# Optimization experiments

Hardware: AMD Instinct MI355X
Metric: run time of the kernel (lower is better)

## Reference

```python
import jax, jax.numpy as jnp
import numpy as np

B, S, D = 8, 2048, 512
EPS = float(jnp.finfo(jnp.float32).eps)  # torch RMSNorm eps=None -> finfo eps


def rmsnorm(x, w):
    var = jnp.mean(jnp.square(x), axis=-1, keepdims=True)
    return x * jax.lax.rsqrt(var + EPS) * w


def setup_inputs() -> dict:
    key = jax.random.key(0)
    ks = jax.random.split(key, 9)
    x = jax.random.normal(ks[0], (B, S, D), dtype=jnp.float32)
    q_expl = jax.random.normal(ks[1], (B, S, D), dtype=jnp.float32)
    k_expl = jax.random.normal(ks[2], (B, S, D), dtype=jnp.float32)
    # parameters (torch Linear: y = x @ W^T + b; store W already transposed [in, out])
    sc1 = 1.0 / np.sqrt(D)
    W1 = jax.random.uniform(ks[3], (D, 2 * D), jnp.float32, -sc1, sc1)
    b1 = jax.random.uniform(ks[4], (2 * D,), jnp.float32, -sc1, sc1)
    W2 = jax.random.uniform(ks[5], (D, D), jnp.float32, -sc1, sc1)
    b2 = jax.random.uniform(ks[6], (D,), jnp.float32, -sc1, sc1)
    norm1_w = jnp.ones((D,), jnp.float32)
    norm2_w = jnp.ones((D,), jnp.float32)
    return {"x": x, "q_expl": q_expl, "k_expl": k_expl,
            "W1": W1, "b1": b1, "W2": W2, "b2": b2,
            "norm1_w": norm1_w, "norm2_w": norm2_w}


def reference(x, q_expl, k_expl, W1, b1, W2, b2, norm1_w, norm2_w):
    d = x.shape[-1]
    # single-head attention: scores [B,S,S]
    scores = jnp.einsum('bqd,bkd->bqk', q_expl, k_expl) / jnp.sqrt(jnp.float32(d))
    attn = jax.nn.softmax(scores, axis=-1)
    attn_out = jnp.einsum('bqk,bkd->bqd', attn, x)
    # dropout is identity in eval mode
    h = rmsnorm(x + attn_out, norm1_w)
    # GeGLU FFN: Linear(D->2D), chunk, gelu(x1)*x2, Linear(D->D)
    proj = h @ W1 + b1
    x1, x2 = jnp.split(proj, 2, axis=-1)
    g = jax.nn.gelu(x1, approximate=False) * x2
    ff = g @ W2 + b2
    return rmsnorm(h + ff, norm2_w)
```

## Files before the change

### kernel.cpp

```cpp
#include <hip/hip_runtime.h>
#include <math.h>

static constexpr float EPS_F = 1.1920929e-07f;
static constexpr float SCL   = 0.044194173824159216f;

typedef __attribute__((ext_vector_type(8))) short  short8;
typedef __attribute__((ext_vector_type(4))) float  floatx4;

__device__ __forceinline__ float4 ld4(const float* p){ return *(const float4*)p; }
__device__ __forceinline__ ushort f2bf(float f){
  union { float f; unsigned u; } v; v.f = f;
  return (ushort)((v.u + 0x7FFFu + ((v.u >> 16) & 1u)) >> 16);
}
__device__ __forceinline__ float bf2f(ushort h){
  union { unsigned u; float f; } v; v.u = ((unsigned)h) << 16;
  return v.f;
}
#define MFMA16(A,B,C) __builtin_amdgcn_mfma_f32_16x16x32_bf16((A),(B),(C),0,0,0)

__device__ __forceinline__ void gld16(void* lds, const void* g){
  __builtin_amdgcn_global_load_lds(
      (const __attribute__((address_space(1))) unsigned int*)g,
      (__attribute__((address_space(3))) unsigned int*)lds, 16, 0, 0);
}


__global__ __launch_bounds__(256)
void prep(const float* __restrict__ q, const float* __restrict__ k,
          const float* __restrict__ x, const float* __restrict__ W1,
          const float* __restrict__ W2,
          ushort* __restrict__ Qb, ushort* __restrict__ Kb,
          ushort* __restrict__ XT, ushort* __restrict__ W1T,
          ushort* __restrict__ W2T)
{
  const int bi = blockIdx.x, t = threadIdx.x;
  if (bi < 8192){
    const size_t i4 = ((size_t)bi*256 + t)*4;
    float4 v = ld4(q + i4);
    ushort4 o;
    o.x=f2bf(v.x*SCL); o.y=f2bf(v.y*SCL); o.z=f2bf(v.z*SCL); o.w=f2bf(v.w*SCL);
    *(ushort4*)(Qb + i4) = o;
    float4 u = ld4(k + i4);
    o.x=f2bf(u.x); o.y=f2bf(u.y); o.z=f2bf(u.z); o.w=f2bf(u.w);
    *(ushort4*)(Kb + i4) = o;
    return;
  }
  const float* in; ushort* out; int R, C, c0, r0; size_t boff;
  if (bi < 10240){
    const int id = bi - 8192;
    in = x; out = XT; R = 2048; C = 512;
    boff = (size_t)(id >> 8) * R * C;
    c0 = (id & 7)*64; r0 = ((id >> 3) & 31)*64;
  } else if (bi < 10368){
    const int id = bi - 10240;
    in = W1; out = W1T; R = 512; C = 1024; boff = 0;
    c0 = (id & 15)*64; r0 = (id >> 4)*64;
  } else {
    const int id = bi - 10368;
    in = W2; out = W2T; R = 512; C = 512; boff = 0;
    c0 = (id & 7)*64; r0 = (id >> 3)*64;
  }
  __shared__ __align__(16) ushort tile[64*68];
#pragma unroll
  for (int it = 0; it < 4; ++it){
    int f = t + it*256, r = f >> 4, c4 = f & 15;
    float4 v = ld4(in + boff + (size_t)(r0+r)*C + c0 + c4*4);
    ushort4 o; o.x=f2bf(v.x); o.y=f2bf(v.y); o.z=f2bf(v.z); o.w=f2bf(v.w);
    *(ushort4*)&tile[r*68 + c4*4] = o;
  }
  __syncthreads();
#pragma unroll
  for (int it = 0; it < 4; ++it){
    int f = t + it*256, c = f >> 4, q4 = f & 15;
    ushort4 o;
    o.x = tile[(q4*4+0)*68 + c];
    o.y = tile[(q4*4+1)*68 + c];
    o.z = tile[(q4*4+2)*68 + c];
    o.w = tile[(q4*4+3)*68 + c];
    *(ushort4*)(out + boff + (size_t)(c0+c)*R + r0 + q4*4) = o;
  }
}

__global__ __launch_bounds__(512)
void qk3(const ushort* __restrict__ Qbf, const ushort* __restrict__ Kbf,
         ushort* __restrict__ scores, float* __restrict__ rowsum)
{
  extern __shared__ __align__(16) ushort smem[];
  const int t = threadIdx.x, lane = t & 63, w = t >> 6;
  const int id = blockIdx.x;
  const int b = id & 7, s = id >> 3;
  const int m0 = (s & 7) * 256, n0 = (s >> 3) * 256;
  const ushort* Ab = Qbf + ((size_t)b*2048 + m0)*512;
  const ushort* Bb = Kbf + ((size_t)b*2048 + n0)*512;
  const int wr = w >> 2, wc = w & 3;
  const int l15 = lane & 15, quad = lane >> 4;
  const int swk = ((l15 >> 1) & 3) * 8;
  const int rl  = lane >> 2;
  const int cl  = (lane & 3) ^ ((lane >> 3) & 3);
  const int aofb = (wr*128 + l15)*32 + (quad*8 ^ swk);
  const int bofb = (wc*64  + l15)*32 + (quad*8 ^ swk);

  floatx4 acc[8][4];
#pragma unroll
  for (int i = 0; i < 8; ++i)
#pragma unroll
    for (int j = 0; j < 4; ++j) acc[i][j] = (floatx4){0.f,0.f,0.f,0.f};

  auto stage = [&](int dstE, const ushort* gsrc, int kt){
#pragma unroll
    for (int r = 0; r < 2; ++r)
      gld16(smem + dstE + w*1024 + r*512,
            gsrc + (size_t)(w*32 + r*16 + rl)*512 + kt*32 + cl*8);
  };

  const int NT = 16;
  stage(0,             Ab, 0);
  stage(16384,         Bb, 0);
  stage(16384 + 8192,  Bb, 1);
  asm volatile("s_waitcnt vmcnt(2)" ::: "memory");
  __builtin_amdgcn_s_barrier();

  short8 af[4], bfr[4];
  for (int kt = 0; kt < NT; ++kt){
    const int cur = kt & 1;
    const ushort* A  = smem + cur*8192;
    const ushort* Bt = smem + 16384 + cur*8192;
#pragma unroll
    for (int n = 0; n < 4; ++n) bfr[n] = *(const short8*)&Bt[bofb + n*512];
#pragma unroll
    for (int m = 0; m < 4; ++m) af[m]  = *(const short8*)&A[aofb + m*512];
    if (kt+1 < NT) stage((cur^1)*8192, Ab, kt+1);
    __builtin_amdgcn_s_barrier();
    asm volatile("s_waitcnt lgkmcnt(0)" ::: "memory");
    __builtin_amdgcn_sched_barrier(0);
    __builtin_amdgcn_s_setprio(1);
#pragma unroll
    for (int m = 0; m < 4; ++m)
#pragma unroll
      for (int n = 0; n < 4; ++n)
        acc[m][n] = MFMA16(af[m], bfr[n], acc[m][n]);
    __builtin_amdgcn_s_setprio(0);
    __builtin_amdgcn_s_barrier();
#pragma unroll
    for (int m = 0; m < 4; ++m) af[m] = *(const short8*)&A[aofb + (4+m)*512];
    if (kt+2 < NT) stage(16384 + cur*8192, Bb, kt+2);
    __builtin_amdgcn_s_barrier();
    asm volatile("s_waitcnt lgkmcnt(0)" ::: "memory");
    __builtin_amdgcn_sched_barrier(0);
    __builtin_amdgcn_s_setprio(1);
#pragma unroll
    for (int m = 0; m < 4; ++m)
#pragma unroll
      for (int n = 0; n < 4; ++n)
        acc[4+m][n] = MFMA16(af[m], bfr[n], acc[4+m][n]);
    __builtin_amdgcn_s_setprio(0);
    if (kt + 2 < NT) asm volatile("s_waitcnt vmcnt(2)" ::: "memory");
    else             asm volatile("s_waitcnt vmcnt(0)" ::: "memory");
    __builtin_amdgcn_s_barrier();
  }

  ushort* sb = scores + (size_t)b*2048*2048;
#pragma unroll
  for (int m = 0; m < 8; ++m){
    const int rm = m0 + wr*128 + m*16 + quad*4;
    float rs[4] = {0.f,0.f,0.f,0.f};
#pragma unroll
    for (int n = 0; n < 4; ++n){
      const int cn = n0 + wc*64 + n*16 + l15;
#pragma unroll
      for (int r = 0; r < 4; ++r){
        float e = __expf(acc[m][n][r]);
        ushort eb = f2bf(e);
        sb[(size_t)(rm + r)*2048 + cn] = eb;
        rs[r] += bf2f(eb);
      }
    }
#pragma unroll
    for (int r = 0; r < 4; ++r){
      float p2 = rs[r];
      p2 += __shfl_xor(p2, 1); p2 += __shfl_xor(p2, 2);
      p2 += __shfl_xor(p2, 4); p2 += __shfl_xor(p2, 8);
      if (l15 == 0)
        atomicAdd(&rowsum[(size_t)b*2048 + rm + r], p2);
    }
  }
}

__global__ __launch_bounds__(512)
void pv8(const ushort* __restrict__ P, const ushort* __restrict__ XT,
         const float* __restrict__ rowsum, ushort* __restrict__ attn)
{
  extern __shared__ __align__(16) ushort smem[];
  const int t = threadIdx.x, lane = t & 63, w = t >> 6;
  const int id = blockIdx.x;
  const int b = id & 7, s = id >> 3;
  const int m0 = (s >> 2) * 256;
  const int n0 = (s & 3) * 128;
  const ushort* Pb = P  + ((size_t)b*2048 + m0)*2048;
  const ushort* Xb = XT + ((size_t)b*512  + n0)*2048;
  const int wr = w >> 1, wc = w & 1;
  const int l15 = lane & 15, quad = lane >> 4;
  const int c0  = (quad ^ (l15 & 7)) * 8;
  const int srow = lane >> 3;
  const int skc  = ((lane & 7) ^ srow) * 8;

  floatx4 acc[4][4];
#pragma unroll
  for (int i = 0; i < 4; ++i)
#pragma unroll
    for (int j = 0; j < 4; ++j) acc[i][j] = (floatx4){0.f,0.f,0.f,0.f};

  auto stageA = [&](int buf, int kt, int h){
    ushort* base = smem + buf*24576 + h*8192;
#pragma unroll
    for (int r = 0; r < 2; ++r){
      const int rw = r*8 + w;
      gld16(base + rw*512,
            Pb + (size_t)(h*128 + rw*8 + srow)*2048 + kt*64 + skc);
    }
  };
  auto stageB = [&](int buf, int kt){
    ushort* base = smem + buf*24576 + 16384;
#pragma unroll
    for (int r = 0; r < 2; ++r){
      const int rw = r*8 + w;
      gld16(base + rw*512,
            Xb + (size_t)(rw*8 + srow)*2048 + kt*64 + skc);
    }
  };

  stageA(0, 0, 0);
  stageA(0, 0, 1);
  stageB(0, 0);
  stageB(1, 1);
  asm volatile("s_waitcnt vmcnt(2)" ::: "memory");
  __builtin_amdgcn_s_barrier();

  short8 af[2][2], bfr[4][2];
  const int NT = 32;

  for (int kt = 0; kt < NT; ++kt){
    const int cur = kt & 1;
    const ushort* A  = smem + cur*24576;
    const ushort* Bt = A + 16384;

#pragma unroll
    for (int ni = 0; ni < 4; ++ni)
#pragma unroll
      for (int ks = 0; ks < 2; ++ks)
        bfr[ni][ks] = *(const short8*)
          &Bt[(wc*64 + ni*16 + l15)*64 + (c0 ^ (ks*32))];
#pragma unroll
    for (int mi = 0; mi < 2; ++mi)
#pragma unroll
      for (int ks = 0; ks < 2; ++ks)
        af[mi][ks] = *(const short8*)
          &A[(wr*64 + mi*16 + l15)*64 + (c0 ^ (ks*32))];
    if (kt+1 < NT) stageA(cur^1, kt+1, 0);
    __builtin_amdgcn_s_barrier();
    asm volatile("s_waitcnt lgkmcnt(0)" ::: "memory");
    __builtin_amdgcn_sched_barrier(0);
    __builtin_amdgcn_s_setprio(1);
#pragma unroll
    for (int mi = 0; mi < 2; ++mi)
#pragma unroll
      for (int ni = 0; ni < 4; ++ni)
#pragma unroll
        for (int ks = 0; ks < 2; ++ks)
          acc[mi][ni] = MFMA16(af[mi][ks], bfr[ni][ks], acc[mi][ni]);
    __builtin_amdgcn_s_setprio(0);
    __builtin_amdgcn_s_barrier();

#pragma unroll
    for (int mi = 0; mi < 2; ++mi)
#pragma unroll
      for (int ks = 0; ks < 2; ++ks)
        af[mi][ks] = *(const short8*)
          &A[(wr*64 + (2+mi)*16 + l15)*64 + (c0 ^ (ks*32))];
    if (kt+1 < NT) stageA(cur^1, kt+1, 1);
    if (kt+2 < NT) stageB(cur, kt+2);
    __builtin_amdgcn_s_barrier();
    asm volatile("s_waitcnt lgkmcnt(0)" ::: "memory");
    __builtin_amdgcn_sched_barrier(0);
    __builtin_amdgcn_s_setprio(1);
#pragma unroll
    for (int mi = 0; mi < 2; ++mi)
#pragma unroll
      for (int ni = 0; ni < 4; ++ni)
#pragma unroll
        for (int ks = 0; ks < 2; ++ks)
          acc[2+mi][ni] = MFMA16(af[mi][ks], bfr[ni][ks], acc[2+mi][ni]);
    __builtin_amdgcn_s_setprio(0);
    if (kt + 2 < NT) asm volatile("s_waitcnt vmcnt(2)" ::: "memory");
    else             asm volatile("s_waitcnt vmcnt(0)" ::: "memory");
    __builtin_amdgcn_s_barrier();
  }

  ushort* ab = attn + (size_t)b*2048*512;
#pragma unroll
  for (int m = 0; m < 4; ++m){
    const int rm = m0 + wr*64 + m*16 + quad*4;
    float inv[4];
#pragma unroll
    for (int r = 0; r < 4; ++r)
      inv[r] = 1.0f / rowsum[(size_t)b*2048 + rm + r];
#pragma unroll
    for (int n = 0; n < 4; ++n){
      const int cn = n0 + wc*64 + n*16 + l15;
#pragma unroll
      for (int r = 0; r < 4; ++r)
        ab[(size_t)(rm + r)*512 + cn] = f2bf(acc[m][n][r] * inv[r]);
    }
  }
}

__global__ __launch_bounds__(256)
void res_rms1(const float* __restrict__ x, const float* __restrict__ n1w,
              ushort* __restrict__ ah)
{
  const int wid = threadIdx.x >> 6, lane = threadIdx.x & 63;
  const size_t row = (size_t)blockIdx.x*4 + wid;
  ushort* ar = ah + row*512;
  const float* xr = x + row*512;
  ushort4 a0 = *(const ushort4*)&ar[lane*8];
  ushort4 a1 = *(const ushort4*)&ar[lane*8 + 4];
  float4 x0 = ld4(xr + lane*8), x1 = ld4(xr + lane*8 + 4);
  float h[8];
  h[0]=x0.x+bf2f(a0.x); h[1]=x0.y+bf2f(a0.y); h[2]=x0.z+bf2f(a0.z); h[3]=x0.w+bf2f(a0.w);
  h[4]=x1.x+bf2f(a1.x); h[5]=x1.y+bf2f(a1.y); h[6]=x1.z+bf2f(a1.z); h[7]=x1.w+bf2f(a1.w);
  float ss = 0.f;
#pragma unroll
  for (int e=0;e<8;++e) ss += h[e]*h[e];
#pragma unroll
  for (int s=1;s<64;s<<=1) ss += __shfl_xor(ss, s);
  const float rr = rsqrtf(ss*(1.0f/512.0f) + EPS_F);
  ushort4 o0, o1;
  o0.x=f2bf(h[0]*rr*n1w[lane*8+0]); o0.y=f2bf(h[1]*rr*n1w[lane*8+1]);
  o0.z=f2bf(h[2]*rr*n1w[lane*8+2]); o0.w=f2bf(h[3]*rr*n1w[lane*8+3]);
  o1.x=f2bf(h[4]*rr*n1w[lane*8+4]); o1.y=f2bf(h[5]*rr*n1w[lane*8+5]);
  o1.z=f2bf(h[6]*rr*n1w[lane*8+6]); o1.w=f2bf(h[7]*rr*n1w[lane*8+7]);
  *(ushort4*)&ar[lane*8]     = o0;
  *(ushort4*)&ar[lane*8 + 4] = o1;
}

__global__ __launch_bounds__(512, 4)
void ffn2(const ushort* __restrict__ hbf, const ushort* __restrict__ W1T,
          const float* __restrict__ b1, ushort* __restrict__ gbuf)
{
  extern __shared__ __align__(16) ushort smem[];
  const int t = threadIdx.x, lane = t & 63, w = t >> 6;
  const int id = blockIdx.x;
  const int xcd = id & 7, sl = id >> 3;
  const int m0 = (xcd*8 + (sl >> 3)) * 256;
  const int n0 = (sl & 7) * 64;
  const ushort* Ab = hbf + (size_t)m0*512;
  const int wr = w >> 1, wc = w & 1;
  const int l15 = lane & 15, quad = lane >> 4;
  const int rl = lane >> 2;
  const int cl = (lane & 3) ^ ((lane >> 3) & 3);
  const int sw = ((l15 >> 1) & 3) * 8;
  int aoff[4], boff[4];
#pragma unroll
  for (int m = 0; m < 4; ++m)
    aoff[m] = ((wr*64 + m*16 + l15)*32 + quad*8) ^ sw;
#pragma unroll
  for (int n = 0; n < 4; ++n)
    boff[n] = ((wc*64 + n*16 + l15)*32 + quad*8) ^ sw;
  const size_t aS0 = (size_t)(w*16 + rl)*512 + cl*8;
  const size_t aS1 = aS0 + (size_t)128*512;
  const int br = w*16 + rl;
  const int bgrow = ((br >> 5) & 1)*512 + n0 + (br >> 6)*32 + (br & 31);
  const size_t bS0 = (size_t)bgrow*512 + cl*8;
  const int aD = w*512, bD = 16384 + w*512;

  floatx4 acc[4][4];
#pragma unroll
  for (int i = 0; i < 4; ++i)
#pragma unroll
    for (int j = 0; j < 4; ++j) acc[i][j] = (floatx4){0.f,0.f,0.f,0.f};

  const int NT = 16;
  gld16(smem + aD,        Ab + aS0);
  gld16(smem + 4096 + aD, Ab + aS1);
  gld16(smem + bD,        W1T + bS0);
  gld16(smem + 4096 + bD, W1T + bS0 + 32);
  asm volatile("s_waitcnt vmcnt(1)" ::: "memory");
  __builtin_amdgcn_s_barrier();

  short8 af[2], bfr[4];
  for (int kt = 0; kt < NT; ++kt){
    const int cur = kt & 1;
    const ushort* A  = smem + cur*8192;
    const ushort* Bt = smem + 16384 + cur*4096;
#pragma unroll
    for (int n = 0; n < 4; ++n) bfr[n] = *(const short8*)&Bt[boff[n]];
#pragma unroll
    for (int m = 0; m < 2; ++m) af[m] = *(const short8*)&A[aoff[m]];
    if (kt+1 < NT){
      ushort* d = smem + (cur^1)*8192;
      const size_t ko = (size_t)(kt+1)*32;
      gld16(d + aD,        Ab + aS0 + ko);
      gld16(d + 4096 + aD, Ab + aS1 + ko);
    }
    __builtin_amdgcn_s_barrier();
    asm volatile("s_waitcnt lgkmcnt(0)" ::: "memory");
    __builtin_amdgcn_sched_barrier(0);
    __builtin_amdgcn_s_setprio(1);
#pragma unroll
    for (int m = 0; m < 2; ++m)
#pragma unroll
      for (int n = 0; n < 4; ++n)
        acc[m][n] = MFMA16(af[m], bfr[n], acc[m][n]);
    __builtin_amdgcn_s_setprio(0);
    __builtin_amdgcn_s_barrier();
#pragma unroll
    for (int m = 0; m < 2; ++m) af[m] = *(const short8*)&A[aoff[2+m]];
    if (kt+2 < NT)
      gld16(smem + cur*4096 + bD, W1T + bS0 + (size_t)(kt+2)*32);
    __builtin_amdgcn_s_barrier();
    asm volatile("s_waitcnt lgkmcnt(0)" ::: "memory");
    __builtin_amdgcn_sched_barrier(0);
    __builtin_amdgcn_s_setprio(1);
#pragma unroll
    for (int m = 0; m < 2; ++m)
#pragma unroll
      for (int n = 0; n < 4; ++n)
        acc[2+m][n] = MFMA16(af[m], bfr[n], acc[2+m][n]);
    __builtin_amdgcn_s_setprio(0);
    if (kt + 2 < NT) asm volatile("s_waitcnt vmcnt(1)" ::: "memory");
    else             asm volatile("s_waitcnt vmcnt(0)" ::: "memory");
    __builtin_amdgcn_s_barrier();
  }

#pragma unroll
  for (int m = 0; m < 4; ++m){
#pragma unroll
    for (int n = 0; n < 2; ++n){
      const int col = n0 + wc*32 + n*16 + l15;
      const float bb1 = b1[col], bb2 = b1[512 + col];
#pragma unroll
      for (int r = 0; r < 4; ++r){
        const int row = m0 + wr*64 + m*16 + quad*4 + r;
        float x1 = acc[m][n][r]     + bb1;
        float x2 = acc[m][n+2][r]   + bb2;
        float gl = 0.5f*x1*(1.0f + erff(x1*0.70710678118654752f));
        gbuf[(size_t)row*512 + col] = f2bf(gl*x2);
      }
    }
  }
}

__global__ __launch_bounds__(512, 4)
void ff2(const ushort* __restrict__ gb, const ushort* __restrict__ W2T,
         ushort* __restrict__ ff)
{
  extern __shared__ __align__(16) ushort smem[];
  const int t = threadIdx.x, lane = t & 63, w = t >> 6;
  const int id = blockIdx.x;
  const int xcd = id & 7, sl = id >> 3;
  const int m0 = (xcd*8 + (sl >> 2)) * 256;
  const int n0 = (sl & 3) * 128;
  const ushort* Ab = gb  + (size_t)m0*512;
  const ushort* Bb = W2T + (size_t)n0*512;
  const int wr = w >> 1, wc = w & 1;
  const int l15 = lane & 15, quad = lane >> 4;
  const int rl = lane >> 2;
  const int cl = (lane & 3) ^ ((lane >> 3) & 3);
  const int sw = ((l15 >> 1) & 3) * 8;
  int aoff[4], boff[4];
#pragma unroll
  for (int m = 0; m < 4; ++m)
    aoff[m] = ((wr*64 + m*16 + l15)*32 + quad*8) ^ sw;
#pragma unroll
  for (int n = 0; n < 4; ++n)
    boff[n] = ((wc*64 + n*16 + l15)*32 + quad*8) ^ sw;
  const size_t aS0 = (size_t)(w*16 + rl)*512 + cl*8;
  const size_t aS1 = aS0 + (size_t)128*512;
  const size_t bS0 = (size_t)(w*16 + rl)*512 + cl*8;
  const int aD = w*512, bD = 16384 + w*512;

  floatx4 acc[4][4];
#pragma unroll
  for (int i = 0; i < 4; ++i)
#pragma unroll
    for (int j = 0; j < 4; ++j) acc[i][j] = (floatx4){0.f,0.f,0.f,0.f};

  const int NT = 16;
  gld16(smem + aD,        Ab + aS0);
  gld16(smem + 4096 + aD, Ab + aS1);
  gld16(smem + bD,        Bb + bS0);
  gld16(smem + 4096 + bD, Bb + bS0 + 32);
  asm volatile("s_waitcnt vmcnt(1)" ::: "memory");
  __builtin_amdgcn_s_barrier();

  short8 af[2], bfr[4];
  for (int kt = 0; kt < NT; ++kt){
    const int cur = kt & 1;
    const ushort* A  = smem + cur*8192;
    const ushort* Bt = smem + 16384 + cur*4096;
#pragma unroll
    for (int n = 0; n < 4; ++n) bfr[n] = *(const short8*)&Bt[boff[n]];
#pragma unroll
    for (int m = 0; m < 2; ++m) af[m] = *(const short8*)&A[aoff[m]];
    if (kt+1 < NT){
      ushort* d = smem + (cur^1)*8192;
      const size_t ko = (size_t)(kt+1)*32;
      gld16(d + aD,        Ab + aS0 + ko);
      gld16(d + 4096 + aD, Ab + aS1 + ko);
    }
    __builtin_amdgcn_s_barrier();
    asm volatile("s_waitcnt lgkmcnt(0)" ::: "memory");
    __builtin_amdgcn_sched_barrier(0);
    __builtin_amdgcn_s_setprio(1);
#pragma unroll
    for (int m = 0; m < 2; ++m)
#pragma unroll
      for (int n = 0; n < 4; ++n)
        acc[m][n] = MFMA16(af[m], bfr[n], acc[m][n]);
    __builtin_amdgcn_s_setprio(0);
    __builtin_amdgcn_s_barrier();
#pragma unroll
    for (int m = 0; m < 2; ++m) af[m] = *(const short8*)&A[aoff[2+m]];
    if (kt+2 < NT)
      gld16(smem + cur*4096 + bD, Bb + bS0 + (size_t)(kt+2)*32);
    __builtin_amdgcn_s_barrier();
    asm volatile("s_waitcnt lgkmcnt(0)" ::: "memory");
    __builtin_amdgcn_sched_barrier(0);
    __builtin_amdgcn_s_setprio(1);
#pragma unroll
    for (int m = 0; m < 2; ++m)
#pragma unroll
      for (int n = 0; n < 4; ++n)
        acc[2+m][n] = MFMA16(af[m], bfr[n], acc[2+m][n]);
    __builtin_amdgcn_s_setprio(0);
    if (kt + 2 < NT) asm volatile("s_waitcnt vmcnt(1)" ::: "memory");
    else             asm volatile("s_waitcnt vmcnt(0)" ::: "memory");
    __builtin_amdgcn_s_barrier();
  }

#pragma unroll
  for (int m = 0; m < 4; ++m){
    const int rm = m0 + wr*64 + m*16 + quad*4;
#pragma unroll
    for (int n = 0; n < 4; ++n){
      const int cn = n0 + wc*64 + n*16 + l15;
#pragma unroll
      for (int r = 0; r < 4; ++r)
        ff[(size_t)(rm + r)*512 + cn] = f2bf(acc[m][n][r]);
    }
  }
}

__global__ __launch_bounds__(256)
void res_rms2(const ushort* __restrict__ hbf, const ushort* __restrict__ ff,
              const float* __restrict__ b2, const float* __restrict__ n2w,
              float* __restrict__ out)
{
  const int wid = threadIdx.x >> 6, lane = threadIdx.x & 63;
  const size_t row = (size_t)blockIdx.x*4 + wid;
  const ushort* hr = hbf + row*512;
  const ushort* fr = ff  + row*512;
  ushort4 h0 = *(const ushort4*)&hr[lane*8];
  ushort4 h1 = *(const ushort4*)&hr[lane*8 + 4];
  ushort4 f0 = *(const ushort4*)&fr[lane*8];
  ushort4 f1 = *(const ushort4*)&fr[lane*8 + 4];
  float4 bb0 = ld4(b2 + lane*8), bb1 = ld4(b2 + lane*8 + 4);
  float y[8];
  y[0]=bf2f(h0.x)+bf2f(f0.x)+bb0.x; y[1]=bf2f(h0.y)+bf2f(f0.y)+bb0.y;
  y[2]=bf2f(h0.z)+bf2f(f0.z)+bb0.z; y[3]=bf2f(h0.w)+bf2f(f0.w)+bb0.w;
  y[4]=bf2f(h1.x)+bf2f(f1.x)+bb1.x; y[5]=bf2f(h1.y)+bf2f(f1.y)+bb1.y;
  y[6]=bf2f(h1.z)+bf2f(f1.z)+bb1.z; y[7]=bf2f(h1.w)+bf2f(f1.w)+bb1.w;
  float ss = 0.f;
#pragma unroll
  for (int e=0;e<8;++e) ss += y[e]*y[e];
#pragma unroll
  for (int s=1;s<64;s<<=1) ss += __shfl_xor(ss, s);
  const float rr = rsqrtf(ss*(1.0f/512.0f) + EPS_F);
  float4 w0 = ld4(n2w + lane*8), w1 = ld4(n2w + lane*8 + 4);
  float* orow = out + row*512;
  float4 o0, o1;
  o0.x=y[0]*rr*w0.x; o0.y=y[1]*rr*w0.y; o0.z=y[2]*rr*w0.z; o0.w=y[3]*rr*w0.w;
  o1.x=y[4]*rr*w1.x; o1.y=y[5]*rr*w1.y; o1.z=y[6]*rr*w1.z; o1.w=y[7]*rr*w1.w;
  *(float4*)(orow + lane*8)     = o0;
  *(float4*)(orow + lane*8 + 4) = o1;
}

extern "C" void kernel_launch(void* const* d_in, const int* in_sizes, int n_in,
                              void* d_out, int out_size, void* d_ws, size_t ws_size,
                              hipStream_t stream)
{
  const float* x   = (const float*)d_in[0];
  const float* q   = (const float*)d_in[1];
  const float* k   = (const float*)d_in[2];
  const float* W1  = (const float*)d_in[3];
  const float* b1  = (const float*)d_in[4];
  const float* W2  = (const float*)d_in[5];
  const float* b2  = (const float*)d_in[6];
  const float* n1w = (const float*)d_in[7];
  const float* n2w = (const float*)d_in[8];
  float* out = (float*)d_out;

  ushort* scoresP = (ushort*)d_ws;
  ushort* XT  = scoresP + (size_t)8*2048*2048;
  ushort* Qbf = XT  + (size_t)8*512*2048;
  ushort* Kbf = Qbf + (size_t)8*2048*512;
  ushort* W1T = Kbf + (size_t)8*2048*512;
  ushort* W2T = W1T + (size_t)1024*512;
  float*  rowsum = (float*)(W2T + (size_t)512*512);
  ushort* attn = Qbf;
  ushort* hbf  = Qbf;
  ushort* gbuf = Kbf;
  ushort* ffb  = scoresP;

  hipMemsetAsync(rowsum, 0, (size_t)8*2048*sizeof(float), stream);
  prep     <<<dim3(10432),  256, 0, stream>>>(q, k, x, W1, W2, Qbf, Kbf, XT, W1T, W2T);
  qk3      <<<dim3(512),    512, 65536, stream>>>(Qbf, Kbf, scoresP, rowsum);
  pv8      <<<dim3(256),    512, 98304, stream>>>(scoresP, XT, rowsum, attn);
  res_rms1 <<<dim3(4096),   256, 0, stream>>>(x, n1w, hbf);
  ffn2     <<<dim3(512),    512, 49152, stream>>>(hbf, W1T, b1, gbuf);
  ff2      <<<dim3(256),    512, 49152, stream>>>(gbuf, W2T, ffb);
  res_rms2 <<<dim3(4096),   256, 0, stream>>>(hbf, ffb, b2, n2w, out);
}
```

Baseline: 302.8 us.

## Retile QK kernel to 256x128 blocks with 64-wide K steps and XOR swizzle

Rewrites the QK^T scores kernel to use 256x128 output tiles per block (1024 blocks instead of 512), a 4x2 wave layout, and 64-element K steps with a new XOR-swizzled shared-memory layout. Each step now issues two MFMAs per fragment pair and halves the number of K iterations, cutting barriers per unit of work. The change doubles the block count and raises LDS to 96KB, which may limit occupancy. It also lowers A/B operand reuse per block, since more Q rows are reloaded across the extra N tiles.

```diff
diff --git a/kernel.cpp b/kernel.cpp
--- a/kernel.cpp
+++ b/kernel.cpp
@@ -82,77 +82,109 @@
 }
 
 __global__ __launch_bounds__(512)
-void qk3(const ushort* __restrict__ Qbf, const ushort* __restrict__ Kbf,
+void qk5(const ushort* __restrict__ Qbf, const ushort* __restrict__ Kbf,
          ushort* __restrict__ scores, float* __restrict__ rowsum)
 {
   extern __shared__ __align__(16) ushort smem[];
   const int t = threadIdx.x, lane = t & 63, w = t >> 6;
   const int id = blockIdx.x;
   const int b = id & 7, s = id >> 3;
-  const int m0 = (s & 7) * 256, n0 = (s >> 3) * 256;
+  const int m0 = (s & 7) * 256;
+  const int n0 = (s >> 3) * 128;
   const ushort* Ab = Qbf + ((size_t)b*2048 + m0)*512;
   const ushort* Bb = Kbf + ((size_t)b*2048 + n0)*512;
-  const int wr = w >> 2, wc = w & 3;
+  const int wr = w >> 1, wc = w & 1;
   const int l15 = lane & 15, quad = lane >> 4;
-  const int swk = ((l15 >> 1) & 3) * 8;
-  const int rl  = lane >> 2;
-  const int cl  = (lane & 3) ^ ((lane >> 3) & 3);
-  const int aofb = (wr*128 + l15)*32 + (quad*8 ^ swk);
-  const int bofb = (wc*64  + l15)*32 + (quad*8 ^ swk);
-
-  floatx4 acc[8][4];
-#pragma unroll
-  for (int i = 0; i < 8; ++i)
+  const int c0  = (quad ^ (l15 & 7)) * 8;
+  const int srow = lane >> 3;
+  const int skc  = ((lane & 7) ^ srow) * 8;
+
+  floatx4 acc[4][4];
+#pragma unroll
+  for (int i = 0; i < 4; ++i)
 #pragma unroll
     for (int j = 0; j < 4; ++j) acc[i][j] = (floatx4){0.f,0.f,0.f,0.f};
 
-  auto stage = [&](int dstE, const ushort* gsrc, int kt){
-#pragma unroll
-    for (int r = 0; r < 2; ++r)
-      gld16(smem + dstE + w*1024 + r*512,
-            gsrc + (size_t)(w*32 + r*16 + rl)*512 + kt*32 + cl*8);
+  auto stageA = [&](int buf, int kt, int h){
+    ushort* base = smem + buf*24576 + h*8192;
+#pragma unroll
+    for (int r = 0; r < 2; ++r){
+      const int rw = r*8 + w;
+      gld16(base + rw*512,
+            Ab + (size_t)(h*128 + rw*8 + srow)*512 + kt*64 + skc);
+    }
   };
-
-  const int NT = 16;
-  stage(0,             Ab, 0);
-  stage(16384,         Bb, 0);
-  stage(16384 + 8192,  Bb, 1);
+  auto stageB = [&](int buf, int kt){
+    ushort* base = smem + buf*24576 + 16384;
+#pragma unroll
+    for (int r = 0; r < 2; ++r){
+      const int rw = r*8 + w;
+      gld16(base + rw*512,
+            Bb + (size_t)(rw*8 + srow)*512 + kt*64 + skc);
+    }
+  };
+
+  stageA(0, 0, 0);
+  stageA(0, 0, 1);
+  stageB(0, 0);
+  stageB(1, 1);
   asm volatile("s_waitcnt vmcnt(2)" ::: "memory");
   __builtin_amdgcn_s_barrier();
 
-  short8 af[4], bfr[4];
+  short8 af[2][2], bfr[4][2];
+  const int NT = 8;
+
   for (int kt = 0; kt < NT; ++kt){
     const int cur = kt & 1;
-    const ushort* A  = smem + cur*8192;
-    const ushort* Bt = smem + 16384 + cur*8192;
-#pragma unroll
-    for (int n = 0; n < 4; ++n) bfr[n] = *(const short8*)&Bt[bofb + n*512];
-#pragma unroll
-    for (int m = 0; m < 4; ++m) af[m]  = *(const short8*)&A[aofb + m*512];
-    if (kt+1 < NT) stage((cur^1)*8192, Ab, kt+1);
-    __builtin_amdgcn_s_barrier();
-    asm volatile("s_waitcnt lgkmcnt(0)" ::: "memory");
-    __builtin_amdgcn_sched_barrier(0);
-    __builtin_amdgcn_s_setprio(1);
-#pragma unroll
-    for (int m = 0; m < 4; ++m)
-#pragma unroll
-      for (int n = 0; n < 4; ++n)
-        acc[m][n] = MFMA16(af[m], bfr[n], acc[m][n]);
-    __builtin_amdgcn_s_setprio(0);
-    __builtin_amdgcn_s_barrier();
-#pragma unroll
-    for (int m = 0; m < 4; ++m) af[m] = *(const short8*)&A[aofb + (4+m)*512];
-    if (kt+2 < NT) stage(16384 + cur*8192, Bb, kt+2);
-    __builtin_amdgcn_s_barrier();
-    asm volatile("s_waitcnt lgkmcnt(0)" ::: "memory");
-    __builtin_amdgcn_sched_barrier(0);
-    __builtin_amdgcn_s_setprio(1);
-#pragma unroll
-    for (int m = 0; m < 4; ++m)
-#pragma unroll
-      for (int n = 0; n < 4; ++n)
-        acc[4+m][n] = MFMA16(af[m], bfr[n], acc[4+m][n]);
+    const ushort* A  = smem + cur*24576;
+    const ushort* Bt = A + 16384;
+
+#pragma unroll
+    for (int ni = 0; ni < 4; ++ni)
+#pragma unroll
+      for (int ks = 0; ks < 2; ++ks)
+        bfr[ni][ks] = *(const short8*)
+          &Bt[(wc*64 + ni*16 + l15)*64 + (c0 ^ (ks*32))];
+#pragma unroll
+    for (int mi = 0; mi < 2; ++mi)
+#pragma unroll
+      for (int ks = 0; ks < 2; ++ks)
+        af[mi][ks] = *(const short8*)
+          &A[(wr*64 + mi*16 + l15)*64 + (c0 ^ (ks*32))];
+    if (kt+1 < NT) stageA(cur^1, kt+1, 0);
+    __builtin_amdgcn_s_barrier();
+    asm volatile("s_waitcnt lgkmcnt(0)" ::: "memory");
+    __builtin_amdgcn_sched_barrier(0);
+    __builtin_amdgcn_s_setprio(1);
+#pragma unroll
+    for (int mi = 0; mi < 2; ++mi)
+#pragma unroll
+      for (int ni = 0; ni < 4; ++ni)
+#pragma unroll
+        for (int ks = 0; ks < 2; ++ks)
+          acc[mi][ni] = MFMA16(af[mi][ks], bfr[ni][ks], acc[mi][ni]);
+    __builtin_amdgcn_s_setprio(0);
+    __builtin_amdgcn_s_barrier();
+
+#pragma unroll
+    for (int mi = 0; mi < 2; ++mi)
+#pragma unroll
+      for (int ks = 0; ks < 2; ++ks)
+        af[mi][ks] = *(const short8*)
+          &A[(wr*64 + (2+mi)*16 + l15)*64 + (c0 ^ (ks*32))];
+    if (kt+1 < NT) stageA(cur^1, kt+1, 1);
+    if (kt+2 < NT) stageB(cur, kt+2);
+    __builtin_amdgcn_s_barrier();
+    asm volatile("s_waitcnt lgkmcnt(0)" ::: "memory");
+    __builtin_amdgcn_sched_barrier(0);
+    __builtin_amdgcn_s_setprio(1);
+#pragma unroll
+    for (int mi = 0; mi < 2; ++mi)
+#pragma unroll
+      for (int ni = 0; ni < 4; ++ni)
+#pragma unroll
+        for (int ks = 0; ks < 2; ++ks)
+          acc[2+mi][ni] = MFMA16(af[mi][ks], bfr[ni][ks], acc[2+mi][ni]);
     __builtin_amdgcn_s_setprio(0);
     if (kt + 2 < NT) asm volatile("s_waitcnt vmcnt(2)" ::: "memory");
     else             asm volatile("s_waitcnt vmcnt(0)" ::: "memory");
@@ -161,8 +193,8 @@
 
   ushort* sb = scores + (size_t)b*2048*2048;
 #pragma unroll
-  for (int m = 0; m < 8; ++m){
-    const int rm = m0 + wr*128 + m*16 + quad*4;
+  for (int m = 0; m < 4; ++m){
+    const int rm = m0 + wr*64 + m*16 + quad*4;
     float rs[4] = {0.f,0.f,0.f,0.f};
 #pragma unroll
     for (int n = 0; n < 4; ++n){
@@ -614,7 +646,7 @@
 
   hipMemsetAsync(rowsum, 0, (size_t)8*2048*sizeof(float), stream);
   prep     <<<dim3(10432),  256, 0, stream>>>(q, k, x, W1, W2, Qbf, Kbf, XT, W1T, W2T);
-  qk3      <<<dim3(512),    512, 65536, stream>>>(Qbf, Kbf, scoresP, rowsum);
+  qk5      <<<dim3(1024),   512, 98304, stream>>>(Qbf, Kbf, scoresP, rowsum);
   pv8      <<<dim3(256),    512, 98304, stream>>>(scoresP, XT, rowsum, attn);
   res_rms1 <<<dim3(4096),   256, 0, stream>>>(x, n1w, hbf);
   ffn2     <<<dim3(512),    512, 49152, stream>>>(hbf, W1T, b1, gbuf);
```

Result: no change. 308.6 us (+1.9%).
